# Kernel tuning notes

Measured on AMD Instinct MI355X. Metric: run time of the kernel, lower is better.

Reference implementation:

```python
import jax, jax.numpy as jnp
import numpy as np

EPS = 1e-5
GROUPS = 8

def _bn(x, g, b, axes):
    # training-mode batch norm over `axes`, channel axis = 1
    m = jnp.mean(x, axis=axes, keepdims=True)
    v = jnp.var(x, axis=axes, keepdims=True)
    shp = (1, -1) + (1,) * (x.ndim - 2)
    return (x - m) / jnp.sqrt(v + EPS) * g.reshape(shp) + b.reshape(shp)

def setup_inputs() -> dict:
    key = jax.random.key(0)
    k0, k1, k2 = jax.random.split(key, 3)
    N, C, T, V = 64, 256, 64, 25
    out_planes = 256
    gp = out_planes // GROUPS  # 32
    x = jax.random.normal(k0, (N, C, T, V), jnp.float32)
    w_qkv = jax.random.normal(k1, (2 * out_planes, C), jnp.float32) * np.float32(np.sqrt(1.0 / C))
    relative = jax.random.normal(k2, (2 * gp, 2 * V - 1), jnp.float32) * np.float32(np.sqrt(1.0 / gp))
    return {
        "x": x,
        "w_qkv": w_qkv,
        "relative": relative,
        "bn_qkv_g": jnp.ones(2 * out_planes, jnp.float32),
        "bn_qkv_b": jnp.zeros(2 * out_planes, jnp.float32),
        "bn_sim_g": jnp.ones(3 * GROUPS, jnp.float32),
        "bn_sim_b": jnp.zeros(3 * GROUPS, jnp.float32),
        "bn_out_g": jnp.ones(2 * out_planes, jnp.float32),
        "bn_out_b": jnp.zeros(2 * out_planes, jnp.float32),
    }

def reference(x, w_qkv, relative, bn_qkv_g, bn_qkv_b, bn_sim_g, bn_sim_b, bn_out_g, bn_out_b):
    N, C, T, V = x.shape
    out_planes = w_qkv.shape[0] // 2
    gp = out_planes // GROUPS
    K = V  # kernel_size == V by construction
    # static relative index table
    qi = np.arange(K)[None, :]
    ki = np.arange(K)[:, None]
    flat_idx = (ki - qi + K - 1).reshape(-1)
    # mean over frames T (permute(0,2,1,3) then mean over dim1 == mean over axis 2)
    y = jnp.mean(x, axis=2)  # [N, C, V]
    # 1x1 conv qkv + BN1d
    qkv = _bn(jnp.einsum('oc,ncv->nov', w_qkv, y), bn_qkv_g, bn_qkv_b, (0, 2))
    qkv = qkv.reshape(N, GROUPS, 2 * gp, V)
    q, k, v = qkv[:, :, : gp // 2], qkv[:, :, gp // 2: gp], qkv[:, :, gp:]
    all_emb = relative[:, flat_idx].reshape(2 * gp, K, K)
    q_e, k_e, v_e = all_emb[: gp // 2], all_emb[gp // 2: gp], all_emb[gp:]
    qr = jnp.einsum('ngci,cij->ngij', q, q_e)
    kr = jnp.einsum('ngci,cij->ngij', k, k_e).swapaxes(2, 3)
    qk = jnp.einsum('ngci,ngcj->ngij', q, k)
    stacked = jnp.concatenate([qk, qr, kr], axis=1)  # [N, 3*groups, V, V]
    stacked = _bn(stacked, bn_sim_g, bn_sim_b, (0, 2, 3)).reshape(N, 3, GROUPS, V, V).sum(axis=1)
    sim = jax.nn.softmax(stacked, axis=3)  # [N, groups, V, V]
    sv = jnp.einsum('ngij,ngcj->ngci', sim, v)
    sve = jnp.einsum('ngij,cij->ngci', sim, v_e)
    so = jnp.concatenate([sv, sve], axis=-1).reshape(N, 2 * out_planes, V)
    o = _bn(so, bn_out_g, bn_out_b, (0, 2)).reshape(N, out_planes, 2, V).sum(axis=2)
    o = jax.nn.sigmoid(o)[:, :, None, :]  # [N, out_planes, 1, V]
    return x + x * o
```

## Files before the change

kernel.cpp:

```cpp
#include <hip/hip_runtime.h>
#include <cmath>

#define NN 64
#define CC 256
#define TT 64
#define VV 25
#define OO 512
#define GG 8
#define NV (NN*VV)
#define STK 625

__global__ __launch_bounds__(256) void k_mean(const float* __restrict__ x,
                                              float* __restrict__ y,
                                              float* __restrict__ accz) {
    __shared__ float tile[TT * VV];
    int b = blockIdx.x;
    if (b == 0) {
        for (int i = threadIdx.x; i < 2096; i += 256) accz[i] = 0.f;
    }
    const float4* x4 = (const float4*)(x + (size_t)b * (TT * VV));
    float4* t4 = (float4*)tile;
    for (int i = threadIdx.x; i < (TT * VV) / 4; i += 256) t4[i] = x4[i];
    __syncthreads();
    if (threadIdx.x < VV) {
        float s = 0.f;
        #pragma unroll
        for (int t = 0; t < TT; ++t) s += tile[t * VV + threadIdx.x];
        y[(size_t)b * VV + threadIdx.x] = s * (1.0f / TT);
    }
}

__global__ __launch_bounds__(256) void k_qkv(const float* __restrict__ y,
                                             const float* __restrict__ w,
                                             float* __restrict__ qkv,
                                             float* __restrict__ qacc) {
    __shared__ float ys[CC][VV + 1];
    __shared__ float qs[64][VV + 1];
    int n = blockIdx.x >> 3, oc = blockIdx.x & 7;
    const float* yp = y + (size_t)n * CC * VV;
    for (int i = threadIdx.x; i < CC * VV; i += 256) ys[i / VV][i % VV] = yp[i];
    __syncthreads();
    int t = threadIdx.x;
    if (t < 200) {
        int v = t % VV, o0 = t / VV;
        const float* wp = w + (size_t)(oc * 64 + o0) * CC;
        float acc[8] = {0, 0, 0, 0, 0, 0, 0, 0};
        for (int c = 0; c < CC; c += 4) {
            float y0 = ys[c][v], y1 = ys[c + 1][v], y2 = ys[c + 2][v], y3 = ys[c + 3][v];
            #pragma unroll
            for (int u = 0; u < 8; ++u) {
                const float4 w4 = *(const float4*)(wp + (size_t)u * 8 * CC + c);
                acc[u] += y0 * w4.x + y1 * w4.y + y2 * w4.z + y3 * w4.w;
            }
        }
        #pragma unroll
        for (int u = 0; u < 8; ++u) qs[o0 + u * 8][v] = acc[u];
    }
    __syncthreads();
    float* qp = qkv + ((size_t)n * OO + oc * 64) * VV;
    for (int i = t; i < 64 * VV; i += 256) qp[i] = qs[i / VV][i % VV];
    if (t < 64) {
        float s = 0.f, s2 = 0.f;
        #pragma unroll
        for (int v = 0; v < VV; ++v) { float val = qs[t][v]; s += val; s2 += val * val; }
        atomicAdd(&qacc[oc * 64 + t], s);
        atomicAdd(&qacc[512 + oc * 64 + t], s2);
    }
}

__global__ __launch_bounds__(256) void k_scores(const float* __restrict__ qkv,
                                                const float* __restrict__ rel,
                                                const float* __restrict__ qacc,
                                                const float* __restrict__ gq,
                                                const float* __restrict__ bq,
                                                float* __restrict__ stk,
                                                float* __restrict__ sacc) {
    int n = blockIdx.x >> 3, gb = blockIdx.x & 7;
    __shared__ float qs[32][VV + 1];
    __shared__ float rs[32 * 49];
    __shared__ float csc[32], csh[32];
    __shared__ float sred[24];
    int t = threadIdx.x;
    if (t < 32) {
        int ch = gb * 64 + t;
        float m = qacc[ch] * (1.0f / NV);
        float var = qacc[512 + ch] * (1.0f / NV) - m * m;
        float sc = gq[ch] * rsqrtf(var + 1e-5f);
        csc[t] = sc; csh[t] = bq[ch] - m * sc;
    }
    __syncthreads();
    for (int i = t; i < 32 * VV; i += 256) {
        int c = i / VV, v = i - c * VV;
        qs[c][v] = qkv[((size_t)n * OO + gb * 64 + c) * VV + v] * csc[c] + csh[c];
    }
    for (int i = t; i < 32 * 49; i += 256) rs[i] = rel[i];
    __syncthreads();
    float ls0 = 0.f, ls1 = 0.f, ls2 = 0.f, ls3 = 0.f, ls4 = 0.f, ls5 = 0.f;
    size_t base = (size_t)n * 24;
    for (int ij = t; ij < STK; ij += 256) {
        int i = ij / VV, j = ij - (ij / VV) * VV;
        float aqk = 0.f, aqr = 0.f, akr = 0.f;
        #pragma unroll
        for (int c = 0; c < 16; ++c) {
            float qv = qs[c][i], kv = qs[16 + c][j];
            aqk += qv * kv;
            aqr += qv * rs[c * 49 + i - j + 24];
            akr += kv * rs[(16 + c) * 49 + j - i + 24];
        }
        stk[(base + gb) * STK + ij]      = aqk;
        stk[(base + 8 + gb) * STK + ij]  = aqr;
        stk[(base + 16 + gb) * STK + ij] = akr;
        ls0 += aqk; ls1 += aqk * aqk;
        ls2 += aqr; ls3 += aqr * aqr;
        ls4 += akr; ls5 += akr * akr;
    }
    #pragma unroll
    for (int off = 32; off > 0; off >>= 1) {
        ls0 += __shfl_down(ls0, off); ls1 += __shfl_down(ls1, off);
        ls2 += __shfl_down(ls2, off); ls3 += __shfl_down(ls3, off);
        ls4 += __shfl_down(ls4, off); ls5 += __shfl_down(ls5, off);
    }
    int lane = t & 63, wid = t >> 6;
    if (lane == 0) {
        sred[wid * 6 + 0] = ls0; sred[wid * 6 + 1] = ls1;
        sred[wid * 6 + 2] = ls2; sred[wid * 6 + 3] = ls3;
        sred[wid * 6 + 4] = ls4; sred[wid * 6 + 5] = ls5;
    }
    __syncthreads();
    if (t < 6) {
        float t2 = sred[t] + sred[6 + t] + sred[12 + t] + sred[18 + t];
        int ch = (t >> 1) * 8 + gb;
        atomicAdd(&sacc[(t & 1) * 24 + ch], t2);
    }
}

__global__ __launch_bounds__(256) void k_attnout(const float* __restrict__ stk,
                                                 const float* __restrict__ qkv,
                                                 const float* __restrict__ rel,
                                                 const float* __restrict__ qacc,
                                                 const float* __restrict__ gq,
                                                 const float* __restrict__ bq,
                                                 const float* __restrict__ sacc,
                                                 const float* __restrict__ gs,
                                                 const float* __restrict__ bs,
                                                 float* __restrict__ so,
                                                 float* __restrict__ oacc) {
    int n = blockIdx.x >> 3, gb = blockIdx.x & 7;
    __shared__ float S[STK];
    __shared__ float vs[32][VV + 1];
    __shared__ float rs[32 * 49];
    __shared__ float svs[800], sves[800];
    __shared__ float csc[32], csh[32];
    __shared__ float simp[6];
    int t = threadIdx.x;
    if (t < 32) {
        int ch = gb * 64 + 32 + t;
        float m = qacc[ch] * (1.0f / NV);
        float var = qacc[512 + ch] * (1.0f / NV) - m * m;
        float sc = gq[ch] * rsqrtf(var + 1e-5f);
        csc[t] = sc; csh[t] = bq[ch] - m * sc;
    }
    if (t < 3) {
        int ch = t * 8 + gb;
        float m = sacc[ch] * (1.0f / 40000.0f);
        float var = sacc[24 + ch] * (1.0f / 40000.0f) - m * m;
        float sc = gs[ch] * rsqrtf(var + 1e-5f);
        simp[t * 2] = sc; simp[t * 2 + 1] = bs[ch] - m * sc;
    }
    __syncthreads();
    const size_t sb = (size_t)n * 24 * STK;
    for (int ij = t; ij < STK; ij += 256)
        S[ij] = stk[sb + (size_t)gb * STK + ij] * simp[0] + simp[1]
              + stk[sb + (size_t)(8 + gb) * STK + ij] * simp[2] + simp[3]
              + stk[sb + (size_t)(16 + gb) * STK + ij] * simp[4] + simp[5];
    for (int i = t; i < 32 * VV; i += 256) {
        int c = i / VV, v = i - (i / VV) * VV;
        vs[c][v] = qkv[((size_t)n * OO + gb * 64 + 32 + c) * VV + v] * csc[c] + csh[c];
    }
    for (int i = t; i < 32 * 49; i += 256) rs[i] = rel[32 * 49 + i];
    __syncthreads();
    if (t < VV) {
        const int i = t;
        float mx = -1e30f;
        #pragma unroll
        for (int j = 0; j < VV; ++j) mx = fmaxf(mx, S[i * VV + j]);
        float e[VV]; float sum = 0.f;
        #pragma unroll
        for (int j = 0; j < VV; ++j) { e[j] = expf(S[i * VV + j] - mx); sum += e[j]; }
        float inv = 1.0f / sum;
        #pragma unroll
        for (int j = 0; j < VV; ++j) S[i * VV + j] = e[j] * inv;
    }
    __syncthreads();
    for (int idx = t; idx < 800; idx += 256) {
        int c = idx / VV, i = idx - (idx / VV) * VV;
        float sv = 0.f, sve = 0.f;
        #pragma unroll
        for (int j = 0; j < VV; ++j) {
            float p = S[i * VV + j];
            sv  += p * vs[c][j];
            sve += p * rs[c * 49 + i - j + 24];
        }
        svs[idx] = sv; sves[idx] = sve;
    }
    __syncthreads();
    if (t < 64) {
        int c = t >> 1;
        const float* src = (t & 1) ? (sves + c * VV) : (svs + c * VV);
        float s = 0.f, s2 = 0.f;
        #pragma unroll
        for (int i = 0; i < VV; ++i) { float val = src[i]; s += val; s2 += val * val; }
        atomicAdd(&oacc[gb * 64 + t], s);
        atomicAdd(&oacc[512 + gb * 64 + t], s2);
    }
    float* sop = so + ((size_t)n * OO + gb * 64) * VV;
    for (int idx = t; idx < 1600; idx += 256) {
        int oc = idx / VV, i = idx - (idx / VV) * VV;
        int c = oc >> 1;
        sop[idx] = (oc & 1) ? sves[c * VV + i] : svs[c * VV + i];
    }
}

__global__ __launch_bounds__(256) void k_final(const float* __restrict__ x,
                                               const float* __restrict__ so,
                                               const float* __restrict__ oacc,
                                               const float* __restrict__ go,
                                               const float* __restrict__ bo,
                                               float* __restrict__ out) {
    int b = blockIdx.x;
    int n = b >> 8, p = b & 255;
    __shared__ float orow[VV];
    if (threadIdx.x < VV) {
        int o0 = 2 * p, o1 = 2 * p + 1;
        float m0 = oacc[o0] * (1.0f / NV);
        float var0 = oacc[512 + o0] * (1.0f / NV) - m0 * m0;
        float sc0 = go[o0] * rsqrtf(var0 + 1e-5f), sh0 = bo[o0] - m0 * sc0;
        float m1 = oacc[o1] * (1.0f / NV);
        float var1 = oacc[512 + o1] * (1.0f / NV) - m1 * m1;
        float sc1 = go[o1] * rsqrtf(var1 + 1e-5f), sh1 = bo[o1] - m1 * sc1;
        int v = threadIdx.x;
        float a  = so[((size_t)n * OO + o0) * VV + v] * sc0 + sh0;
        float c2 = so[((size_t)n * OO + o1) * VV + v] * sc1 + sh1;
        float z = a + c2;
        orow[v] = 1.0f + 1.0f / (1.0f + expf(-z));
    }
    __syncthreads();
    const float4* x4 = (const float4*)(x + (size_t)b * (TT * VV));
    float4* y4 = (float4*)(out + (size_t)b * (TT * VV));
    for (int wv = threadIdx.x; wv < (TT * VV) / 4; wv += 256) {
        float4 xv = x4[wv];
        int e = 4 * wv;
        int v0 = e % VV;
        float4 r;
        int v;
        v = v0;                      r.x = xv.x * orow[v];
        v = v0 + 1; if (v >= VV) v -= VV; r.y = xv.y * orow[v];
        v = v0 + 2; if (v >= VV) v -= VV; r.z = xv.z * orow[v];
        v = v0 + 3; if (v >= VV) v -= VV; r.w = xv.w * orow[v];
        y4[wv] = r;
    }
}

extern "C" void kernel_launch(void* const* d_in, const int* in_sizes, int n_in,
                              void* d_out, int out_size, void* d_ws, size_t ws_size,
                              hipStream_t stream) {
    (void)in_sizes; (void)n_in; (void)out_size; (void)ws_size;
    const float* x        = (const float*)d_in[0];
    const float* w_qkv    = (const float*)d_in[1];
    const float* relative = (const float*)d_in[2];
    const float* bn_qkv_g = (const float*)d_in[3];
    const float* bn_qkv_b = (const float*)d_in[4];
    const float* bn_sim_g = (const float*)d_in[5];
    const float* bn_sim_b = (const float*)d_in[6];
    const float* bn_out_g = (const float*)d_in[7];
    const float* bn_out_b = (const float*)d_in[8];
    float* out = (float*)d_out;

    float* ws = (float*)d_ws;
    float* w_y    = ws;
    float* w_qkvp = ws + 409600;
    float* w_stk  = ws + 1228800;
    float* w_so   = ws + 2188800;
    float* qacc   = ws + 3008000;
    float* sacc   = qacc + 1024;
    float* oacc   = sacc + 48;

    k_mean<<<NN * CC, 256, 0, stream>>>(x, w_y, qacc);
    k_qkv<<<NN * 8, 256, 0, stream>>>(w_y, w_qkv, w_qkvp, qacc);
    k_scores<<<NN * GG, 256, 0, stream>>>(w_qkvp, relative, qacc, bn_qkv_g, bn_qkv_b, w_stk, sacc);
    k_attnout<<<NN * GG, 256, 0, stream>>>(w_stk, w_qkvp, relative, qacc, bn_qkv_g, bn_qkv_b,
                                           sacc, bn_sim_g, bn_sim_b, w_so, oacc);
    k_final<<<NN * CC, 256, 0, stream>>>(x, w_so, oacc, bn_out_g, bn_out_b, out);
}
```

Measured before the change: 277.5 us.

## Parallelize mean and softmax reductions, widen qkv loop, reverse final block order

k_mean now spreads the sum over frames across 200 threads with a shared partial-sum stage, where before 25 threads each did the full 64-frame loop. The scores softmax uses 8 lanes per row with shuffle reductions, and the qkv GEMV loop is unrolled to 8 channels per iteration. k_final walks its blocks in reverse so the most recently touched x data may still be in cache, and it uses nontemporal loads and stores for the streaming output. These are several unrelated micro-optimizations, and the reversed order and nontemporal hints may interact with cache in ways that are hard to predict.

```diff
diff --git a/kernel.cpp b/kernel.cpp
--- a/kernel.cpp
+++ b/kernel.cpp
@@ -10,10 +10,13 @@
 #define NV (NN*VV)
 #define STK 625
 
+typedef float f4 __attribute__((ext_vector_type(4)));
+
 __global__ __launch_bounds__(256) void k_mean(const float* __restrict__ x,
                                               float* __restrict__ y,
                                               float* __restrict__ accz) {
     __shared__ float tile[TT * VV];
+    __shared__ float part[8][VV];
     int b = blockIdx.x;
     if (b == 0) {
         for (int i = threadIdx.x; i < 2096; i += 256) accz[i] = 0.f;
@@ -22,11 +25,20 @@
     float4* t4 = (float4*)tile;
     for (int i = threadIdx.x; i < (TT * VV) / 4; i += 256) t4[i] = x4[i];
     __syncthreads();
-    if (threadIdx.x < VV) {
+    int t = threadIdx.x;
+    if (t < 200) {
+        int v = t % VV, ch = t / VV;
         float s = 0.f;
         #pragma unroll
-        for (int t = 0; t < TT; ++t) s += tile[t * VV + threadIdx.x];
-        y[(size_t)b * VV + threadIdx.x] = s * (1.0f / TT);
+        for (int k = 0; k < 8; ++k) s += tile[(ch * 8 + k) * VV + v];
+        part[ch][v] = s;
+    }
+    __syncthreads();
+    if (t < VV) {
+        float s = 0.f;
+        #pragma unroll
+        for (int k = 0; k < 8; ++k) s += part[k][t];
+        y[(size_t)b * VV + t] = s * (1.0f / TT);
     }
 }
 
@@ -45,12 +57,15 @@
         int v = t % VV, o0 = t / VV;
         const float* wp = w + (size_t)(oc * 64 + o0) * CC;
         float acc[8] = {0, 0, 0, 0, 0, 0, 0, 0};
-        for (int c = 0; c < CC; c += 4) {
-            float y0 = ys[c][v], y1 = ys[c + 1][v], y2 = ys[c + 2][v], y3 = ys[c + 3][v];
+        for (int c = 0; c < CC; c += 8) {
+            float y0 = ys[c][v],     y1 = ys[c + 1][v], y2 = ys[c + 2][v], y3 = ys[c + 3][v];
+            float y4_ = ys[c + 4][v], y5 = ys[c + 5][v], y6 = ys[c + 6][v], y7 = ys[c + 7][v];
             #pragma unroll
             for (int u = 0; u < 8; ++u) {
-                const float4 w4 = *(const float4*)(wp + (size_t)u * 8 * CC + c);
-                acc[u] += y0 * w4.x + y1 * w4.y + y2 * w4.z + y3 * w4.w;
+                const float4 wa = *(const float4*)(wp + (size_t)u * 8 * CC + c);
+                const float4 wb = *(const float4*)(wp + (size_t)u * 8 * CC + c + 4);
+                acc[u] += y0 * wa.x + y1 * wa.y + y2 * wa.z + y3 * wa.w
+                        + y4_ * wb.x + y5 * wb.y + y6 * wb.z + y7 * wb.w;
             }
         }
         #pragma unroll
@@ -179,17 +194,22 @@
     }
     for (int i = t; i < 32 * 49; i += 256) rs[i] = rel[32 * 49 + i];
     __syncthreads();
-    if (t < VV) {
-        const int i = t;
+    if (t < 200) {
+        int i = t >> 3, l = t & 7;
         float mx = -1e30f;
-        #pragma unroll
-        for (int j = 0; j < VV; ++j) mx = fmaxf(mx, S[i * VV + j]);
-        float e[VV]; float sum = 0.f;
-        #pragma unroll
-        for (int j = 0; j < VV; ++j) { e[j] = expf(S[i * VV + j] - mx); sum += e[j]; }
+        for (int j = l; j < VV; j += 8) mx = fmaxf(mx, S[i * VV + j]);
+        #pragma unroll
+        for (int off = 4; off > 0; off >>= 1) mx = fmaxf(mx, __shfl_xor(mx, off));
+        float sum = 0.f;
+        for (int j = l; j < VV; j += 8) {
+            float e = expf(S[i * VV + j] - mx);
+            S[i * VV + j] = e;
+            sum += e;
+        }
+        #pragma unroll
+        for (int off = 4; off > 0; off >>= 1) sum += __shfl_xor(sum, off);
         float inv = 1.0f / sum;
-        #pragma unroll
-        for (int j = 0; j < VV; ++j) S[i * VV + j] = e[j] * inv;
+        for (int j = l; j < VV; j += 8) S[i * VV + j] *= inv;
     }
     __syncthreads();
     for (int idx = t; idx < 800; idx += 256) {
@@ -227,7 +247,7 @@
                                                const float* __restrict__ go,
                                                const float* __restrict__ bo,
                                                float* __restrict__ out) {
-    int b = blockIdx.x;
+    int b = (NN * CC - 1) - blockIdx.x;
     int n = b >> 8, p = b & 255;
     __shared__ float orow[VV];
     if (threadIdx.x < VV) {
@@ -245,19 +265,19 @@
         orow[v] = 1.0f + 1.0f / (1.0f + expf(-z));
     }
     __syncthreads();
-    const float4* x4 = (const float4*)(x + (size_t)b * (TT * VV));
-    float4* y4 = (float4*)(out + (size_t)b * (TT * VV));
+    const f4* x4 = (const f4*)(x + (size_t)b * (TT * VV));
+    f4* y4 = (f4*)(out + (size_t)b * (TT * VV));
     for (int wv = threadIdx.x; wv < (TT * VV) / 4; wv += 256) {
-        float4 xv = x4[wv];
+        f4 xv = __builtin_nontemporal_load(&x4[wv]);
         int e = 4 * wv;
         int v0 = e % VV;
-        float4 r;
+        f4 r;
         int v;
         v = v0;                      r.x = xv.x * orow[v];
         v = v0 + 1; if (v >= VV) v -= VV; r.y = xv.y * orow[v];
         v = v0 + 2; if (v >= VV) v -= VV; r.z = xv.z * orow[v];
         v = v0 + 3; if (v >= VV) v -= VV; r.w = xv.w * orow[v];
-        y4[wv] = r;
+        __builtin_nontemporal_store(r, &y4[wv]);
     }
 }
 
```

Measured after the change: 277.0 us. No clear change (-0.2%).
